# Kernel optimization log

Measured on AMD Instinct MI355X. Metric: run time of the kernel, lower is better.

The kernel has to match this reference:

```python
import jax
import jax.numpy as jnp
from jax import lax
import numpy as np

N_LAYER = 8
SCALE = 4
H_CH = 128
Z_CH = 64


def conv2d(x, w, b=None, stride=1, pad=0):
    # x: NCHW, w: OIHW
    out = lax.conv_general_dilated(
        x, w, (stride, stride), [(pad, pad), (pad, pad)],
        dimension_numbers=("NCHW", "OIHW", "NCHW"))
    if b is not None:
        out = out + b[None, :, None, None]
    return out


def conv_transpose2d(x, w, stride):
    # torch ConvTranspose2d semantics, weight shape (in, out, kH, kW), no bias
    return lax.conv_transpose(
        x, w, (stride, stride), "VALID",
        dimension_numbers=("NCHW", "IOHW", "NCHW"), transpose_kernel=True)


def lstm_cell(inp, hidden, cell, gw, gb, tw, tb):
    # inp = inp + transform(hidden); gates fused into one conv (order f,i,o,s)
    inp = inp + conv2d(hidden, tw, tb, pad=2)
    gates = conv2d(inp, gw, gb, pad=2)
    f, i, o, s = jnp.split(gates, 4, axis=1)
    cell = jax.nn.sigmoid(f) * cell + jax.nn.sigmoid(i) * jnp.tanh(s)
    hidden = jax.nn.sigmoid(o) * jnp.tanh(cell)
    return hidden, cell


def setup_inputs() -> dict:
    key = jax.random.key(0)
    ks = jax.random.split(key, 24)
    b, xc, H, W = 64, 3, 64, 64
    vd, rd = 7, 256
    hs, ws = H // SCALE, W // SCALE
    enc_in = vd + rd + xc + H_CH   # 394
    dec_in = vd + rd + Z_CH        # 327

    def w_init(k, shape):
        fan_in = int(np.prod(shape[1:]))
        return jax.random.normal(k, shape, jnp.float32) / np.sqrt(fan_in)

    inp = {
        "x": jax.random.normal(ks[0], (b, xc, H, W), jnp.float32),
        "v": jax.random.normal(ks[1], (b, vd), jnp.float32),
        "r": jax.random.normal(ks[2], (b, rd, hs, ws), jnp.float32),
        "eps": jax.random.normal(ks[3], (N_LAYER, b, Z_CH, hs, ws), jnp.float32),
        "read_w": w_init(ks[4], (xc, xc, SCALE, SCALE)),
        "write_w": w_init(ks[5], (H_CH, H_CH, SCALE, SCALE)),  # (in,out,kH,kW)
        "prior_w": w_init(ks[6], (2 * Z_CH, H_CH, 5, 5)),
        "prior_b": jnp.zeros((2 * Z_CH,), jnp.float32),
        "post_w": w_init(ks[7], (2 * Z_CH, H_CH, 5, 5)),
        "post_b": jnp.zeros((2 * Z_CH,), jnp.float32),
        "enc_gw": w_init(ks[8], (4 * H_CH, enc_in, 5, 5)),
        "enc_gb": jnp.zeros((4 * H_CH,), jnp.float32),
        "enc_tw": w_init(ks[9], (enc_in, H_CH, 5, 5)),
        "enc_tb": jnp.zeros((enc_in,), jnp.float32),
        "dec_gw": w_init(ks[10], (4 * H_CH, dec_in, 5, 5)),
        "dec_gb": jnp.zeros((4 * H_CH,), jnp.float32),
        "dec_tw": w_init(ks[11], (dec_in, H_CH, 5, 5)),
        "dec_tb": jnp.zeros((dec_in,), jnp.float32),
        "obs_w": w_init(ks[12], (xc, H_CH, 1, 1)),
        "obs_b": jnp.zeros((xc,), jnp.float32),
    }
    return inp


def reference(x, v, r, eps, read_w, write_w, prior_w, prior_b, post_w, post_b,
              enc_gw, enc_gb, enc_tw, enc_tb, dec_gw, dec_gb, dec_tw, dec_tb,
              obs_w, obs_b):
    b, _, H, W = x.shape
    hs, ws = H // SCALE, W // SCALE
    dt = x.dtype
    h_enc = jnp.zeros((b, H_CH, hs, ws), dt)
    c_enc = jnp.zeros((b, H_CH, hs, ws), dt)
    h_dec = jnp.zeros((b, H_CH, hs, ws), dt)
    c_dec = jnp.zeros((b, H_CH, hs, ws), dt)
    u = jnp.zeros((b, H_CH, H, W), dt)

    xr = conv2d(x, read_w, stride=SCALE)            # (b, xc, hs, ws)
    vb = jnp.broadcast_to(v[:, :, None, None], (b, v.shape[1], hs, ws))
    rb = r if r.shape[2] == hs else jnp.tile(r, (1, 1, hs, ws))

    kl_loss = jnp.zeros((), dt)
    for t in range(N_LAYER):
        p_mu, p_lv = jnp.split(conv2d(h_dec, prior_w, prior_b, pad=2), 2, axis=1)
        h_enc, c_enc = lstm_cell(
            jnp.concatenate([h_dec, xr, vb, rb], axis=1),
            h_enc, c_enc, enc_gw, enc_gb, enc_tw, enc_tb)
        q_mu, q_lv = jnp.split(conv2d(h_enc, post_w, post_b, pad=2), 2, axis=1)
        z = q_mu + jnp.exp(0.5 * q_lv) * eps[t]
        h_dec, c_dec = lstm_cell(
            jnp.concatenate([z, vb, rb], axis=1),
            h_dec, c_dec, dec_gw, dec_gb, dec_tw, dec_tb)
        u = u + conv_transpose2d(h_dec, write_w, SCALE)
        # KL(q||p) with var = exp(logvar); log(var1/var0) = p_lv - q_lv
        kl = 0.5 * (jnp.exp(q_lv - p_lv)
                    + (p_mu - q_mu) ** 2 * jnp.exp(-p_lv)
                    - 1.0 + (p_lv - q_lv))
        kl_loss = kl_loss + kl.sum(axis=(1, 2, 3)).mean()

    canvas = jax.nn.sigmoid(conv2d(u, obs_w, obs_b))
    return canvas, kl_loss
```

## Files before the change

kernel.cpp:

```cpp
#include <hip/hip_runtime.h>
#include <hip/hip_bf16.h>

using bf16 = __hip_bfloat16;
typedef __attribute__((ext_vector_type(8))) short short8;
typedef __attribute__((ext_vector_type(4))) short s16x4;
typedef __attribute__((ext_vector_type(4))) float f32x4;
typedef __attribute__((ext_vector_type(8))) int i32x8;
typedef __attribute__((ext_vector_type(4))) int i32x4;
typedef __attribute__((ext_vector_type(2))) int i32x2;

#define DEVI __device__ __forceinline__

#define MTOT 16384
#define PADS 25600

DEVI float sigm_(float x){ return 1.f/(1.f+expf(-x)); }

DEVI float s2f(short v){
  unsigned u = ((unsigned)(unsigned short)v) << 16;
  return __builtin_bit_cast(float, u);
}
DEVI short f2s(float x){
  bf16 hb = __float2bfloat16(x);
  return __builtin_bit_cast(short, hb);
}

DEVI long pidx_(int m){
  int nb = m>>8, iy=(m>>4)&15, ix=m&15;
  return (long)(nb*20 + iy + 2)*20 + (ix + 2);
}

DEVI unsigned char f2fp8(float x){
  int p = __builtin_amdgcn_cvt_pk_fp8_f32(x, 0.f, 0, false);
  return (unsigned char)(p & 0xFF);
}
DEVI float fp82f(unsigned char v){
  return __builtin_amdgcn_cvt_f32_fp8((int)v, 0);
}
DEVI unsigned pack4fp8(float a, float b, float c, float d){
  int w = __builtin_amdgcn_cvt_pk_fp8_f32(a, b, 0, false);
  w     = __builtin_amdgcn_cvt_pk_fp8_f32(c, d, w, true);
  return (unsigned)w;
}

DEVI void async16(const void* g, void* l) {
  __builtin_amdgcn_global_load_lds(
      (__attribute__((address_space(1))) void*)(unsigned long long)g,
      (__attribute__((address_space(3))) void*)(unsigned int)(unsigned long long)l,
      16, 0, 0);
}

template<int CA, int NSF>
DEVI void g8_core(const unsigned char* __restrict__ A8,
                  const unsigned char* __restrict__ Bt8,
                  int m0, int n0, unsigned char* AsB, unsigned char* BsB,
                  f32x4 (&acc)[4][4], int ns0, int nst)
{
  constexpr int Kp8 = NSF*128;
  const int tid = threadIdx.x;
  const int wv = tid>>6, ln = tid&63;

  const int rr = tid>>3;
  const int lc = (tid&7) ^ (rr&7);
  long paRC[4], pbR[4];
  #pragma unroll
  for (int i=0;i<4;i++){
    int m = m0 + rr + (i<<5);
    paRC[i] = (long)(((m>>8)*20 + ((m>>4)&15))*20 + (m&15)) * CA;
    pbR[i]  = (long)(n0 + rr + (i<<5))*Kp8 + lc*16;
  }

  int cc = lc*16, tp = ns0, ks = ns0*128;
  auto stage = [&](int d){
    const int shiftC = ((tp/5)*20 + (tp%5)) * CA;
    char* la = (char*)AsB + d*16384 + (wv<<10);
    char* lb = (char*)BsB + d*16384 + (wv<<10);
    #pragma unroll
    for (int i=0;i<4;i++) async16(A8 + paRC[i] + shiftC + cc, la + i*4096);
    #pragma unroll
    for (int i=0;i<4;i++) async16(Bt8 + pbR[i] + ks, lb + i*4096);
    cc += 128; if (cc >= CA){ cc -= CA; tp++; }
    ks += 128;
  };

  const int wm = wv>>1, wn = wv&1;
  const int rA0 = (wm<<6) + (ln&15);
  const int rB0 = (wn<<6) + (ln&15);
  const int xa = ln&7;
  const int q2 = (ln>>4)<<1;
  const int c0 = ((q2    ) ^ xa)<<4;
  const int c1 = ((q2 | 1) ^ xa)<<4;

  stage(0);
  for (int t=0; t<nst; ++t) {
    asm volatile("s_waitcnt vmcnt(0)\ns_barrier" ::: "memory");
    if (t+1 < nst) stage((t+1)&1);

    const char* as_ = (const char*)AsB + (t&1)*16384;
    const char* bs_ = (const char*)BsB + (t&1)*16384;
    i32x8 af[4], bfr[4];
    #pragma unroll
    for (int f=0; f<4; f++){
      const char* p = as_ + ((rA0 + (f<<4))<<7);
      ((i32x4*)&af[f])[0] = *(const i32x4*)(p + c0);
      ((i32x4*)&af[f])[1] = *(const i32x4*)(p + c1);
    }
    #pragma unroll
    for (int f=0; f<4; f++){
      const char* p = bs_ + ((rB0 + (f<<4))<<7);
      ((i32x4*)&bfr[f])[0] = *(const i32x4*)(p + c0);
      ((i32x4*)&bfr[f])[1] = *(const i32x4*)(p + c1);
    }
    __builtin_amdgcn_s_setprio(1);
    #pragma unroll
    for (int bf=0; bf<4; bf++)
      #pragma unroll
      for (int afi=0; afi<4; afi++)
        acc[bf][afi] = __builtin_amdgcn_mfma_scale_f32_16x16x128_f8f6f4(
            bfr[bf], af[afi], acc[bf][afi], 0, 0, 0, 122, 0, 127);
    __builtin_amdgcn_s_setprio(0);
  }
}

template<int CA, int NS>
__global__ __launch_bounds__(256)
void conv_g8(const unsigned char* __restrict__ A8,
             const unsigned char* __restrict__ Bt8,
             const float* __restrict__ bias, bf16* __restrict__ outB)
{
  __shared__ alignas(16) unsigned char As[2][16384];
  __shared__ alignas(16) unsigned char Bs[2][16384];
  const int m0 = blockIdx.x<<7, n0 = blockIdx.y<<7;
  f32x4 acc[4][4] = {};
  g8_core<CA,NS>(A8, Bt8, m0, n0, &As[0][0], &Bs[0][0], acc, 0, NS);

  const int tid = threadIdx.x;
  const int wv = tid>>6, ln = tid&63;
  const int mb = m0 + ((wv>>1)<<6);
  const int nb = n0 + ((wv&1)<<6);
  const int ml = (ln>>4)<<2;
  const int nl = ln&15;
  #pragma unroll
  for (int bf=0; bf<4; bf++)
    #pragma unroll
    for (int afi=0; afi<4; afi++) {
      const long m = mb + (afi<<4) + nl;
      const int n = nb + (bf<<4) + ml;
      f32x4 b = *(const f32x4*)(bias + n);
      f32x4 v = acc[bf][afi];
      s16x4 o;
      #pragma unroll
      for (int j=0;j<4;j++) o[j] = f2s(v[j] + b[j]);
      *(s16x4*)(outB + (m<<9) + n) = o;
    }
}

__global__ __launch_bounds__(256)
void conv_tp8(const unsigned char* __restrict__ h8Dec,
              const unsigned char* __restrict__ h8Enc,
              const unsigned char* __restrict__ Bt8DP,
              const unsigned char* __restrict__ Bt8EncT,
              const float* __restrict__ TBD, const float* __restrict__ prior_b,
              const float* __restrict__ TBE,
              float* __restrict__ PriorO,
              unsigned char* __restrict__ sDec8, const bf16* __restrict__ STdec,
              unsigned char* __restrict__ sEnc8, const bf16* __restrict__ STenc,
              const bf16* __restrict__ hDecB)
{
  __shared__ alignas(16) unsigned char As[2][16384];
  __shared__ alignas(16) unsigned char Bs[2][16384];
  const int z = blockIdx.z;
  const int m0 = blockIdx.x<<7, n0 = blockIdx.y<<7;
  f32x4 acc[4][4] = {};
  if (z == 0) g8_core<128,25>(h8Dec, Bt8DP,   m0, n0, &As[0][0], &Bs[0][0], acc, 0, 25);
  else        g8_core<128,25>(h8Enc, Bt8EncT, m0, n0, &As[0][0], &Bs[0][0], acc, 0, 25);

  const int tid = threadIdx.x;
  const int wv = tid>>6, ln = tid&63;
  const int mb = m0 + ((wv>>1)<<6);
  const int nb = n0 + ((wv&1)<<6);
  const int ml = (ln>>4)<<2;
  const int nl = ln&15;
  #pragma unroll
  for (int afi=0; afi<4; afi++) {
    const long m = mb + (afi<<4) + nl;
    const long pI = pidx_(m);
    #pragma unroll
    for (int bf=0; bf<4; bf++) {
      const int n = nb + (bf<<4) + ml;
      f32x4 v = acc[bf][afi];
      if (z == 0) {
        if (n0 == 384) {
          f32x4 b = *(const f32x4*)(prior_b + (n-384));
          *(f32x4*)(PriorO + (m<<7) + (n-384)) = v + b;
        } else if (n < 352) {
          f32x4 tb = *(const f32x4*)(TBD + n);
          s16x4 st = *(const s16x4*)(STdec + m*352 + n);
          float f0 = v[0]+tb[0]+s2f(st[0]);
          float f1 = v[1]+tb[1]+s2f(st[1]);
          float f2 = v[2]+tb[2]+s2f(st[2]);
          float f3 = v[3]+tb[3]+s2f(st[3]);
          *(unsigned*)(sDec8 + pI*352 + n) = pack4fp8(f0,f1,f2,f3);
        }
      } else {
        if (n < 416) {
          f32x4 tb = *(const f32x4*)(TBE + n);
          s16x4 st = *(const s16x4*)(STenc + m*416 + n);
          float f0 = v[0]+tb[0]+s2f(st[0]);
          float f1 = v[1]+tb[1]+s2f(st[1]);
          float f2 = v[2]+tb[2]+s2f(st[2]);
          float f3 = v[3]+tb[3]+s2f(st[3]);
          if (n < 128) {
            s16x4 e = *(const s16x4*)(hDecB + (pI<<7) + n);
            f0 += s2f(e[0]); f1 += s2f(e[1]); f2 += s2f(e[2]); f3 += s2f(e[3]);
          }
          *(unsigned*)(sEnc8 + pI*416 + n) = pack4fp8(f0,f1,f2,f3);
        }
      }
    }
  }
}

__global__ __launch_bounds__(256)
void conv_p8(const unsigned char* __restrict__ h8Enc,
             const unsigned char* __restrict__ Bt8Post,
             bf16* __restrict__ PP)
{
  __shared__ alignas(16) unsigned char As[2][16384];
  __shared__ alignas(16) unsigned char Bs[2][16384];
  const int z = blockIdx.z;
  const int s0[4]  = {0, 7, 13, 19};
  const int len[4] = {7, 6, 6, 6};
  const int m0 = blockIdx.x<<7;
  f32x4 acc[4][4] = {};
  g8_core<128,25>(h8Enc, Bt8Post, m0, 0, &As[0][0], &Bs[0][0], acc, s0[z], len[z]);

  bf16* plane = PP + (long)z*MTOT*128;
  const int tid = threadIdx.x;
  const int wv = tid>>6, ln = tid&63;
  const int mb = m0 + ((wv>>1)<<6);
  const int nb = (wv&1)<<6;
  const int ml = (ln>>4)<<2;
  const int nl = ln&15;
  #pragma unroll
  for (int bf=0; bf<4; bf++)
    #pragma unroll
    for (int afi=0; afi<4; afi++) {
      const long m = mb + (afi<<4) + nl;
      const int n = nb + (bf<<4) + ml;
      f32x4 v = acc[bf][afi];
      s16x4 o;
      #pragma unroll
      for (int j=0;j<4;j++) o[j] = f2s(v[j]);
      *(s16x4*)(plane + (m<<7) + n) = o;
    }
}

__global__ void repack_w8_k(const float* __restrict__ w, unsigned char* __restrict__ Bt,
                            int O, int I, int CA, int Kp8, long total)
{
  long e = (long)blockIdx.x*256 + threadIdx.x;
  if (e >= total) return;
  int o = (int)(e / Kp8);
  int k = (int)(e % Kp8);
  float v = 0.f;
  if (k < 25*CA) {
    int blk = k / CA, c = k % CA;
    if (o < O && c < I) v = w[((long)o*I + c)*25 + blk] * 32.0f;
  }
  Bt[e] = f2fp8(v);
}

__global__ void padbias_k(const float* __restrict__ etb, const float* __restrict__ dtb,
                          float* __restrict__ tbe, float* __restrict__ tbd)
{
  int i = threadIdx.x;
  if (i < 416) tbe[i] = (i < 394) ? etb[i] : 0.f;
  if (i < 352) tbd[i] = (i < 327) ? dtb[i] : 0.f;
}

__global__ void wcomb_k(const float* __restrict__ ww, const float* __restrict__ ow,
                        float* __restrict__ Wc)
{
  int idx = blockIdx.x*256 + threadIdx.x;
  if (idx >= 128*48) return;
  int c = idx / 48, rst = idx % 48;
  int pix = rst / 3, o = rst % 3;
  int ki = pix >> 2, kj = pix & 3;
  float a = 0.f;
  for (int mm=0; mm<128; mm++)
    a += ww[(((long)c*128 + mm)*4 + ki)*4 + kj] * ow[o*128 + mm];
  Wc[idx] = a;
}

__global__ void xr_k(const float* __restrict__ x, const float* __restrict__ rw,
                     float* __restrict__ xr)
{
  int idx = blockIdx.x*256 + threadIdx.x;
  if (idx >= MTOT*3) return;
  int m = idx / 3, o = idx % 3;
  int nb = m>>8, iy=(m>>4)&15, ix=m&15;
  float a = 0.f;
  for (int c=0;c<3;c++)
    for (int kh=0;kh<4;kh++)
      for (int kw=0;kw<4;kw++)
        a += x[((long)(nb*3+c)*64 + (iy*4+kh))*64 + (ix*4+kw)] * rw[((o*3+c)*4+kh)*4+kw];
  xr[idx] = a;
}

__global__ void st_enc_k(const float* __restrict__ xr, const float* __restrict__ v,
                         const float* __restrict__ r, bf16* __restrict__ ST)
{
  long g = (long)blockIdx.x*256 + threadIdx.x;
  if (g >= (long)MTOT*266) return;
  int m = (int)(g / 266), ch = (int)(g % 266);
  int nb = m>>8, sp = m&255;
  float val;
  if (ch < 3)       val = xr[m*3 + ch];
  else if (ch < 10) val = v[nb*7 + ch - 3];
  else              val = r[((long)nb*256 + (ch-10))*256 + sp];
  ST[(long)m*416 + 128 + ch] = __float2bfloat16(val);
}

__global__ void st_dec_k(const float* __restrict__ v, const float* __restrict__ r,
                         bf16* __restrict__ ST)
{
  long g = (long)blockIdx.x*256 + threadIdx.x;
  if (g >= (long)MTOT*263) return;
  int m = (int)(g / 263), ch = (int)(g % 263);
  int nb = m>>8, sp = m&255;
  float val;
  if (ch < 7) val = v[nb*7 + ch];
  else        val = r[((long)nb*256 + (ch-7))*256 + sp];
  ST[(long)m*352 + 64 + ch] = __float2bfloat16(val);
}

template<bool SB>
DEVI void lstm8_(const bf16* __restrict__ gates, float* __restrict__ cbuf,
                 bf16* __restrict__ hpad, unsigned char* __restrict__ h8,
                 int m, int c0, float* hout)
{
  long gb = ((long)m<<9) + c0;
  short8 gf = *(const short8*)(gates + gb);
  short8 gi = *(const short8*)(gates + gb + 128);
  short8 go = *(const short8*)(gates + gb + 256);
  short8 gs = *(const short8*)(gates + gb + 384);
  float* cb = cbuf + ((long)m<<7) + c0;
  f32x4 cv0 = *(f32x4*)cb;
  f32x4 cv1 = *(f32x4*)(cb+4);
  short8 hh;
  #pragma unroll
  for (int j=0;j<8;j++){
    float f = s2f(gf[j]);
    float i = s2f(gi[j]);
    float o = s2f(go[j]);
    float s = s2f(gs[j]);
    float cell = sigm_(f)*((j<4)?cv0[j]:cv1[j-4]) + sigm_(i)*tanhf(s);
    if (j<4) cv0[j]=cell; else cv1[j-4]=cell;
    float h = sigm_(o)*tanhf(cell);
    hout[j] = h;
    if constexpr (SB) hh[j] = f2s(h);
  }
  *(f32x4*)cb = cv0;
  *(f32x4*)(cb+4) = cv1;
  long hp = (pidx_(m)<<7) + c0;
  if constexpr (SB) *(short8*)(hpad + hp) = hh;
  int w0 = __builtin_amdgcn_cvt_pk_fp8_f32(hout[0], hout[1], 0, false);
  w0 = __builtin_amdgcn_cvt_pk_fp8_f32(hout[2], hout[3], w0, true);
  int w1 = __builtin_amdgcn_cvt_pk_fp8_f32(hout[4], hout[5], 0, false);
  w1 = __builtin_amdgcn_cvt_pk_fp8_f32(hout[6], hout[7], w1, true);
  i32x2 pw; pw[0]=w0; pw[1]=w1;
  *(i32x2*)(h8 + hp) = pw;
}

__global__ __launch_bounds__(256)
void lstm_k(const bf16* __restrict__ gates, float* __restrict__ cbuf,
            unsigned char* __restrict__ h8)
{
  const int tid = threadIdx.x;
  const int m = (blockIdx.x<<4) + (tid>>4);
  const int c0 = (tid&15)<<3;
  float h[8];
  lstm8_<false>(gates, cbuf, nullptr, h8, m, c0, h);
}

__global__ __launch_bounds__(256)
void lstm_wrc_k(const bf16* __restrict__ gates, float* __restrict__ cbuf,
                bf16* __restrict__ hpad, unsigned char* __restrict__ h8,
                const float* __restrict__ Wc, float* __restrict__ uc)
{
  __shared__ float Wl[6144];
  __shared__ float hl[16*128];
  const int tid = threadIdx.x;
  for (int i = tid; i < 6144; i += 256) Wl[i] = Wc[i];
  const int mloc = tid>>4;
  const int m = (blockIdx.x<<4) + mloc;
  const int c0 = (tid&15)<<3;
  float h[8];
  lstm8_<true>(gates, cbuf, hpad, h8, m, c0, h);
  #pragma unroll
  for (int j=0;j<8;j++) hl[(mloc<<7) + c0 + j] = h[j];
  __syncthreads();

  const int pix = tid&15;
  const float* hrow = hl + (mloc<<7);
  float a0=0.f, a1=0.f, a2=0.f;
  #pragma unroll 4
  for (int c=0;c<128;c++) {
    float hv = hrow[c];
    const float* wl = Wl + c*48 + pix*3;
    a0 += hv*wl[0]; a1 += hv*wl[1]; a2 += hv*wl[2];
  }
  const int nb = m>>8, iy=(m>>4)&15, ix=m&15;
  const int ki = pix>>2, kj = pix&3;
  long ob = ((long)((nb<<6) + (iy<<2) + ki)*64 + (ix<<2) + kj)*3;
  uc[ob+0] += a0; uc[ob+1] += a1; uc[ob+2] += a2;
}

__global__ void zkl4_k(const bf16* __restrict__ PP, const float* __restrict__ pb,
                       const float* __restrict__ prior, const float* __restrict__ eps_t,
                       unsigned char* __restrict__ sDec8, float* __restrict__ part)
{
  __shared__ float wsum[4];
  const long PL = (long)MTOT*128;
  int idx = blockIdx.x*256 + threadIdx.x;
  int m = idx >> 6, c = idx & 63;
  float qm = pb[c], ql = pb[64 + c];
  #pragma unroll
  for (int z=0; z<4; ++z) {
    qm += __bfloat162float(PP[z*PL + ((long)m<<7) + c]);
    ql += __bfloat162float(PP[z*PL + ((long)m<<7) + 64 + c]);
  }
  long pbx = (long)m << 7;
  float pm = prior[pbx + c], pl = prior[pbx + 64 + c];
  int nb = m>>8, sp = m&255;
  float e = eps_t[((long)nb*64 + c)*256 + sp];
  float z = qm + expf(0.5f*ql)*e;
  long so = pidx_(m)*352 + c;
  sDec8[so] = f2fp8(fp82f(sDec8[so]) + z);
  float kl = expf(ql - pl) + (pm-qm)*(pm-qm)*expf(-pl) - 1.f + (pl - ql);
  #pragma unroll
  for (int off=32; off>0; off>>=1) kl += __shfl_down(kl, off);
  if ((threadIdx.x & 63) == 0) wsum[threadIdx.x >> 6] = kl;
  __syncthreads();
  if (threadIdx.x == 0)
    part[blockIdx.x] = wsum[0] + wsum[1] + wsum[2] + wsum[3];
}

__global__ void canvas_k(const float* __restrict__ uc, const float* __restrict__ ob,
                         float* __restrict__ out)
{
  int idx = blockIdx.x*256 + threadIdx.x;
  int x = idx & 63, y = (idx>>6)&63;
  int rem = idx >> 12;
  int o = rem % 3, n = rem / 3;
  float v = uc[((long)((n<<6)+y)*64 + x)*3 + o] + ob[o];
  out[idx] = 1.f/(1.f+expf(-v));
}

__global__ void klred_k(const float* __restrict__ part, float* __restrict__ out)
{
  __shared__ float wsum[4];
  float a = 0.f;
  for (int i = threadIdx.x; i < 32768; i += 256) a += part[i];
  #pragma unroll
  for (int off=32; off>0; off>>=1) a += __shfl_down(a, off);
  if ((threadIdx.x & 63) == 0) wsum[threadIdx.x >> 6] = a;
  __syncthreads();
  if (threadIdx.x == 0)
    out[786432] = (wsum[0] + wsum[1] + wsum[2] + wsum[3]) * (0.5f/64.f);
}

static const long O_BT_POST  = 0;
static const long O_BT_ENCT  = O_BT_POST  + 819200;
static const long O_BT_DP    = O_BT_ENCT  + 3276800;
static const long O_BT_ENCG  = O_BT_DP    + 3276800;
static const long O_BT_DECG  = O_BT_ENCG  + 10649600;
static const long O_WCOMB    = O_BT_DECG  + 9011200;
static const long O_XR       = O_WCOMB    + 24576;
static const long O_KLP      = O_XR       + 196608;
static const long O_STENC    = O_KLP      + 131072;
static const long O_STDEC    = O_STENC    + 13631488;
static const long O_HENC     = O_STDEC    + 11534336;
static const long O_HDEC     = O_HENC     + 6553600;
static const long O_SENC     = O_HDEC     + 6553600;
static const long O_SDEC     = O_SENC     + 21299200;
static const long O_CENC     = O_SDEC     + 18022400;
static const long O_CDEC     = O_CENC     + 8388608;
static const long O_PRIOR    = O_CDEC     + 8388608;
static const long O_H8E      = O_PRIOR    + 8388608;
static const long O_H8D      = O_H8E      + 3276800;
static const long O_PG       = O_H8D      + 3276800;
static const long O_UC       = O_PG       + 33554432;
static const long O_TBE      = O_UC       + 3145728;
static const long O_TBD      = O_TBE      + 2048;
static const long WS_TOTAL   = O_TBD      + 2048;

extern "C" void kernel_launch(void* const* d_in, const int* in_sizes, int n_in,
                              void* d_out, int out_size, void* d_ws, size_t ws_size,
                              hipStream_t stream)
{
  const float* x       = (const float*)d_in[0];
  const float* v       = (const float*)d_in[1];
  const float* r       = (const float*)d_in[2];
  const float* eps     = (const float*)d_in[3];
  const float* read_w  = (const float*)d_in[4];
  const float* write_w = (const float*)d_in[5];
  const float* prior_w = (const float*)d_in[6];
  const float* prior_b = (const float*)d_in[7];
  const float* post_w  = (const float*)d_in[8];
  const float* post_b  = (const float*)d_in[9];
  const float* enc_gw  = (const float*)d_in[10];
  const float* enc_gb  = (const float*)d_in[11];
  const float* enc_tw  = (const float*)d_in[12];
  const float* enc_tb  = (const float*)d_in[13];
  const float* dec_gw  = (const float*)d_in[14];
  const float* dec_gb  = (const float*)d_in[15];
  const float* dec_tw  = (const float*)d_in[16];
  const float* dec_tb  = (const float*)d_in[17];
  const float* obs_w   = (const float*)d_in[18];
  const float* obs_b   = (const float*)d_in[19];

  char* ws = (char*)d_ws;
  unsigned char* Bt8Post = (unsigned char*)(ws + O_BT_POST);
  unsigned char* Bt8EncT = (unsigned char*)(ws + O_BT_ENCT);
  unsigned char* Bt8DP   = (unsigned char*)(ws + O_BT_DP);
  unsigned char* Bt8EncG = (unsigned char*)(ws + O_BT_ENCG);
  unsigned char* Bt8DecG = (unsigned char*)(ws + O_BT_DECG);
  float* Wcomb  = (float*)(ws + O_WCOMB);
  float* XR     = (float*)(ws + O_XR);
  float* KLpart = (float*)(ws + O_KLP);
  bf16* STenc   = (bf16*)(ws + O_STENC);
  bf16* STdec   = (bf16*)(ws + O_STDEC);
  bf16* hDec    = (bf16*)(ws + O_HDEC);
  unsigned char* sEnc8 = (unsigned char*)(ws + O_SENC);
  unsigned char* sDec8 = (unsigned char*)(ws + O_SDEC);
  float* cEnc   = (float*)(ws + O_CENC);
  float* cDec   = (float*)(ws + O_CDEC);
  float* PriorO = (float*)(ws + O_PRIOR);
  unsigned char* h8Enc = (unsigned char*)(ws + O_H8E);
  unsigned char* h8Dec = (unsigned char*)(ws + O_H8D);
  bf16* Gates   = (bf16*)(ws + O_PG);
  bf16* PostP   = (bf16*)(ws + O_PG + 16777216);
  float* Ucomb  = (float*)(ws + O_UC);
  float* TBE    = (float*)(ws + O_TBE);
  float* TBD    = (float*)(ws + O_TBD);
  float* out    = (float*)d_out;

  size_t clr = (size_t)WS_TOTAL; if (clr > ws_size) clr = ws_size;
  hipMemsetAsync(d_ws, 0, clr, stream);

  repack_w8_k<<<1600, 256, 0, stream>>>(post_w, Bt8Post, 128, 128, 128, 3200, 128L*3200);
  repack_w8_k<<<6400, 256, 0, stream>>>(enc_tw, Bt8EncT, 394, 128, 128, 3200, 512L*3200);
  repack_w8_k<<<4800, 256, 0, stream>>>(dec_tw, Bt8DP, 327, 128, 128, 3200, 384L*3200);
  repack_w8_k<<<1600, 256, 0, stream>>>(prior_w, Bt8DP + 384L*3200, 128, 128, 128, 3200, 128L*3200);
  repack_w8_k<<<20992, 256, 0, stream>>>(enc_gw, Bt8EncG, 512, 394, 416, 82*128, 512L*10496);
  repack_w8_k<<<17664, 256, 0, stream>>>(dec_gw, Bt8DecG, 512, 327, 352, 69*128, 512L*8832);
  padbias_k<<<1, 512, 0, stream>>>(enc_tb, dec_tb, TBE, TBD);
  wcomb_k<<<24, 256, 0, stream>>>(write_w, obs_w, Wcomb);
  xr_k<<<192, 256, 0, stream>>>(x, read_w, XR);
  st_enc_k<<<(int)(((long)MTOT*266 + 255)/256), 256, 0, stream>>>(XR, v, r, STenc);
  st_dec_k<<<(int)(((long)MTOT*263 + 255)/256), 256, 0, stream>>>(v, r, STdec);

  for (int t = 0; t < 8; ++t) {
    conv_tp8<<<dim3(128,4,2), 256, 0, stream>>>(
        h8Dec, h8Enc, Bt8DP, Bt8EncT, TBD, prior_b, TBE,
        PriorO, sDec8, STdec, sEnc8, STenc, hDec);
    conv_g8<416,82><<<dim3(128,4), 256, 0, stream>>>(sEnc8, Bt8EncG, enc_gb, Gates);
    lstm_k<<<1024, 256, 0, stream>>>(Gates, cEnc, h8Enc);
    conv_p8<<<dim3(128,1,4), 256, 0, stream>>>(h8Enc, Bt8Post, PostP);
    zkl4_k<<<4096, 256, 0, stream>>>(PostP, post_b, PriorO,
                                     eps + (long)t*64*64*256, sDec8,
                                     KLpart + (long)t*4096);
    conv_g8<352,69><<<dim3(128,4), 256, 0, stream>>>(sDec8, Bt8DecG, dec_gb, Gates);
    lstm_wrc_k<<<1024, 256, 0, stream>>>(Gates, cDec, hDec, h8Dec, Wcomb, Ucomb);
  }

  canvas_k<<<3072, 256, 0, stream>>>(Ucomb, obs_b, out);
  klred_k<<<1, 256, 0, stream>>>(KLpart, out);
}
```

Before: 2.516 ms.

## Restructure fp8 conv K-loop by kernel rows and use fragment-ordered LDS layout

Reorganizes the implicit-GEMM K dimension per kernel row (kw*CA contiguous, padded to 128 multiples) instead of per tap. A stage can now span tap boundaries within a row, which slightly changes the K padding for the gate convs (416*5 padded to 17*128 per row). The global-to-LDS copies are reordered so that each wave's MFMA fragments are stored contiguously, replacing the XOR-swizzled row reads with linear lane-strided ds_reads. The aim is cheaper address arithmetic, fewer wasted K steps, and conflict-free LDS reads. In exchange, the global loads become less coalesced, and the weights repack has to match the new K ordering.

```diff
diff --git a/kernel.cpp b/kernel.cpp
--- a/kernel.cpp
+++ b/kernel.cpp
@@ -50,66 +50,62 @@
       16, 0, 0);
 }
 
-template<int CA, int NSF>
+template<int CA, int NROW>
 DEVI void g8_core(const unsigned char* __restrict__ A8,
                   const unsigned char* __restrict__ Bt8,
                   int m0, int n0, unsigned char* AsB, unsigned char* BsB,
                   f32x4 (&acc)[4][4], int ns0, int nst)
 {
-  constexpr int Kp8 = NSF*128;
+  constexpr int Kp8 = 5*NROW*128;
   const int tid = threadIdx.x;
   const int wv = tid>>6, ln = tid&63;
 
-  const int rr = tid>>3;
-  const int lc = (tid&7) ^ (rr&7);
-  long paRC[4], pbR[4];
+  long paA[4], pbB[4];
   #pragma unroll
   for (int i=0;i<4;i++){
-    int m = m0 + rr + (i<<5);
-    paRC[i] = (long)(((m>>8)*20 + ((m>>4)&15))*20 + (m&15)) * CA;
-    pbR[i]  = (long)(n0 + rr + (i<<5))*Kp8 + lc*16;
-  }
-
-  int cc = lc*16, tp = ns0, ks = ns0*128;
+    const int p = tid + (i<<8);
+    const int H = p>>9, blk = (p>>6)&7, pl = p&63;
+    const int trow = (H<<6) + ((blk>>1)<<4) + (pl&15);
+    const int kch = ((pl>>4)<<1) + (blk&1);
+    const int mA = m0 + trow;
+    paA[i] = (long)(((mA>>8)*20 + ((mA>>4)&15))*20 + (mA&15))*CA + kch*16;
+    pbB[i] = (long)(n0 + trow)*Kp8 + kch*16;
+  }
+
+  int rowc = ns0 % NROW;
+  long sh = (long)(ns0/NROW)*20*CA + (long)rowc*128;
+  long ks = (long)ns0*128;
+
   auto stage = [&](int d){
-    const int shiftC = ((tp/5)*20 + (tp%5)) * CA;
     char* la = (char*)AsB + d*16384 + (wv<<10);
     char* lb = (char*)BsB + d*16384 + (wv<<10);
     #pragma unroll
-    for (int i=0;i<4;i++) async16(A8 + paRC[i] + shiftC + cc, la + i*4096);
-    #pragma unroll
-    for (int i=0;i<4;i++) async16(Bt8 + pbR[i] + ks, lb + i*4096);
-    cc += 128; if (cc >= CA){ cc -= CA; tp++; }
+    for (int i=0;i<4;i++) async16(A8 + paA[i] + sh, la + i*4096);
+    #pragma unroll
+    for (int i=0;i<4;i++) async16(Bt8 + pbB[i] + ks, lb + i*4096);
     ks += 128;
+    sh += 128;
+    if (++rowc == NROW){ rowc = 0; sh += 20*CA - NROW*128; }
   };
 
   const int wm = wv>>1, wn = wv&1;
-  const int rA0 = (wm<<6) + (ln&15);
-  const int rB0 = (wn<<6) + (ln&15);
-  const int xa = ln&7;
-  const int q2 = (ln>>4)<<1;
-  const int c0 = ((q2    ) ^ xa)<<4;
-  const int c1 = ((q2 | 1) ^ xa)<<4;
+  const char* ra = (const char*)AsB + (wm<<13) + (ln<<4);
+  const char* rb = (const char*)BsB + (wn<<13) + (ln<<4);
 
   stage(0);
   for (int t=0; t<nst; ++t) {
     asm volatile("s_waitcnt vmcnt(0)\ns_barrier" ::: "memory");
     if (t+1 < nst) stage((t+1)&1);
 
-    const char* as_ = (const char*)AsB + (t&1)*16384;
-    const char* bs_ = (const char*)BsB + (t&1)*16384;
+    const char* as_ = ra + (t&1)*16384;
+    const char* bs_ = rb + (t&1)*16384;
     i32x8 af[4], bfr[4];
     #pragma unroll
     for (int f=0; f<4; f++){
-      const char* p = as_ + ((rA0 + (f<<4))<<7);
-      ((i32x4*)&af[f])[0] = *(const i32x4*)(p + c0);
-      ((i32x4*)&af[f])[1] = *(const i32x4*)(p + c1);
-    }
-    #pragma unroll
-    for (int f=0; f<4; f++){
-      const char* p = bs_ + ((rB0 + (f<<4))<<7);
-      ((i32x4*)&bfr[f])[0] = *(const i32x4*)(p + c0);
-      ((i32x4*)&bfr[f])[1] = *(const i32x4*)(p + c1);
+      ((i32x4*)&af[f])[0]  = *(const i32x4*)(as_ + (f*2  )*1024);
+      ((i32x4*)&af[f])[1]  = *(const i32x4*)(as_ + (f*2+1)*1024);
+      ((i32x4*)&bfr[f])[0] = *(const i32x4*)(bs_ + (f*2  )*1024);
+      ((i32x4*)&bfr[f])[1] = *(const i32x4*)(bs_ + (f*2+1)*1024);
     }
     __builtin_amdgcn_s_setprio(1);
     #pragma unroll
@@ -122,7 +118,7 @@
   }
 }
 
-template<int CA, int NS>
+template<int CA, int NROW>
 __global__ __launch_bounds__(256)
 void conv_g8(const unsigned char* __restrict__ A8,
              const unsigned char* __restrict__ Bt8,
@@ -132,7 +128,7 @@
   __shared__ alignas(16) unsigned char Bs[2][16384];
   const int m0 = blockIdx.x<<7, n0 = blockIdx.y<<7;
   f32x4 acc[4][4] = {};
-  g8_core<CA,NS>(A8, Bt8, m0, n0, &As[0][0], &Bs[0][0], acc, 0, NS);
+  g8_core<CA,NROW>(A8, Bt8, m0, n0, &As[0][0], &Bs[0][0], acc, 0, 5*NROW);
 
   const int tid = threadIdx.x;
   const int wv = tid>>6, ln = tid&63;
@@ -172,8 +168,8 @@
   const int z = blockIdx.z;
   const int m0 = blockIdx.x<<7, n0 = blockIdx.y<<7;
   f32x4 acc[4][4] = {};
-  if (z == 0) g8_core<128,25>(h8Dec, Bt8DP,   m0, n0, &As[0][0], &Bs[0][0], acc, 0, 25);
-  else        g8_core<128,25>(h8Enc, Bt8EncT, m0, n0, &As[0][0], &Bs[0][0], acc, 0, 25);
+  if (z == 0) g8_core<128,5>(h8Dec, Bt8DP,   m0, n0, &As[0][0], &Bs[0][0], acc, 0, 25);
+  else        g8_core<128,5>(h8Enc, Bt8EncT, m0, n0, &As[0][0], &Bs[0][0], acc, 0, 25);
 
   const int tid = threadIdx.x;
   const int wv = tid>>6, ln = tid&63;
@@ -233,7 +229,7 @@
   const int len[4] = {7, 6, 6, 6};
   const int m0 = blockIdx.x<<7;
   f32x4 acc[4][4] = {};
-  g8_core<128,25>(h8Enc, Bt8Post, m0, 0, &As[0][0], &Bs[0][0], acc, s0[z], len[z]);
+  g8_core<128,5>(h8Enc, Bt8Post, m0, 0, &As[0][0], &Bs[0][0], acc, s0[z], len[z]);
 
   bf16* plane = PP + (long)z*MTOT*128;
   const int tid = threadIdx.x;
@@ -257,16 +253,19 @@
 }
 
 __global__ void repack_w8_k(const float* __restrict__ w, unsigned char* __restrict__ Bt,
-                            int O, int I, int CA, int Kp8, long total)
+                            int O, int I, int CA, int NROW, long total)
 {
   long e = (long)blockIdx.x*256 + threadIdx.x;
   if (e >= total) return;
+  const int RW = NROW*128;
+  const int Kp8 = 5*RW;
   int o = (int)(e / Kp8);
   int k = (int)(e % Kp8);
+  int kh = k / RW, r = k - kh*RW;
   float v = 0.f;
-  if (k < 25*CA) {
-    int blk = k / CA, c = k % CA;
-    if (o < O && c < I) v = w[((long)o*I + c)*25 + blk] * 32.0f;
+  if (r < 5*CA) {
+    int kw = r / CA, c = r % CA;
+    if (o < O && c < I) v = w[((long)o*I + c)*25 + kh*5 + kw] * 32.0f;
   }
   Bt[e] = f2fp8(v);
 }
@@ -550,12 +549,12 @@
   size_t clr = (size_t)WS_TOTAL; if (clr > ws_size) clr = ws_size;
   hipMemsetAsync(d_ws, 0, clr, stream);
 
-  repack_w8_k<<<1600, 256, 0, stream>>>(post_w, Bt8Post, 128, 128, 128, 3200, 128L*3200);
-  repack_w8_k<<<6400, 256, 0, stream>>>(enc_tw, Bt8EncT, 394, 128, 128, 3200, 512L*3200);
-  repack_w8_k<<<4800, 256, 0, stream>>>(dec_tw, Bt8DP, 327, 128, 128, 3200, 384L*3200);
-  repack_w8_k<<<1600, 256, 0, stream>>>(prior_w, Bt8DP + 384L*3200, 128, 128, 128, 3200, 128L*3200);
-  repack_w8_k<<<20992, 256, 0, stream>>>(enc_gw, Bt8EncG, 512, 394, 416, 82*128, 512L*10496);
-  repack_w8_k<<<17664, 256, 0, stream>>>(dec_gw, Bt8DecG, 512, 327, 352, 69*128, 512L*8832);
+  repack_w8_k<<<1600, 256, 0, stream>>>(post_w, Bt8Post, 128, 128, 128, 5, 128L*3200);
+  repack_w8_k<<<6400, 256, 0, stream>>>(enc_tw, Bt8EncT, 394, 128, 128, 5, 512L*3200);
+  repack_w8_k<<<4800, 256, 0, stream>>>(dec_tw, Bt8DP, 327, 128, 128, 5, 384L*3200);
+  repack_w8_k<<<1600, 256, 0, stream>>>(prior_w, Bt8DP + 384L*3200, 128, 128, 128, 5, 128L*3200);
+  repack_w8_k<<<21760, 256, 0, stream>>>(enc_gw, Bt8EncG, 512, 394, 416, 17, 512L*10880);
+  repack_w8_k<<<17920, 256, 0, stream>>>(dec_gw, Bt8DecG, 512, 327, 352, 14, 512L*8960);
   padbias_k<<<1, 512, 0, stream>>>(enc_tb, dec_tb, TBE, TBD);
   wcomb_k<<<24, 256, 0, stream>>>(write_w, obs_w, Wcomb);
   xr_k<<<192, 256, 0, stream>>>(x, read_w, XR);
@@ -566,13 +565,13 @@
     conv_tp8<<<dim3(128,4,2), 256, 0, stream>>>(
         h8Dec, h8Enc, Bt8DP, Bt8EncT, TBD, prior_b, TBE,
         PriorO, sDec8, STdec, sEnc8, STenc, hDec);
-    conv_g8<416,82><<<dim3(128,4), 256, 0, stream>>>(sEnc8, Bt8EncG, enc_gb, Gates);
+    conv_g8<416,17><<<dim3(128,4), 256, 0, stream>>>(sEnc8, Bt8EncG, enc_gb, Gates);
     lstm_k<<<1024, 256, 0, stream>>>(Gates, cEnc, h8Enc);
     conv_p8<<<dim3(128,1,4), 256, 0, stream>>>(h8Enc, Bt8Post, PostP);
     zkl4_k<<<4096, 256, 0, stream>>>(PostP, post_b, PriorO,
                                      eps + (long)t*64*64*256, sDec8,
                                      KLpart + (long)t*4096);
-    conv_g8<352,69><<<dim3(128,4), 256, 0, stream>>>(sDec8, Bt8DecG, dec_gb, Gates);
+    conv_g8<352,14><<<dim3(128,4), 256, 0, stream>>>(sDec8, Bt8DecG, dec_gb, Gates);
     lstm_wrc_k<<<1024, 256, 0, stream>>>(Gates, cDec, hDec, h8Dec, Wcomb, Ucomb);
   }
 
```

Result: slower. 3.355 ms (+33.4%).
